# Kernel optimization log

Measured on AMD Instinct MI355X. Metric: run time of the kernel, lower is better.

The kernel has to match this reference:

```python
import jax, jax.numpy as jnp
import numpy as np

HID = 2048
NH = 16
HD = HID // NH  # 128
EPS = 1e-6
BASE = 10000.0


def _rmsnorm(x, w):
    xf = x.astype(jnp.float32)
    y = xf * jax.lax.rsqrt(jnp.mean(xf * xf, axis=-1, keepdims=True) + EPS)
    return y.astype(x.dtype) * w


def _rope_cos_sin(seq_len, dtype):
    inv_freq = 1.0 / (BASE ** (jnp.arange(0, HD, 2, dtype=jnp.float32) / HD))
    t = jnp.arange(seq_len, dtype=jnp.float32)
    freqs = jnp.outer(t, inv_freq)          # [S, HD/2]
    emb = jnp.concatenate([freqs, freqs], axis=-1)  # [S, HD]
    return jnp.cos(emb).astype(dtype), jnp.sin(emb).astype(dtype)


def _rotate_half(x):
    x1, x2 = jnp.split(x, 2, axis=-1)
    return jnp.concatenate([-x2, x1], axis=-1)


def setup_inputs() -> dict:
    key = jax.random.key(0)
    ks = jax.random.split(key, 8)
    B, S = 2, 2048
    s = 0.02
    return {
        "hidden_states": jax.random.normal(ks[0], (B, S, HID), jnp.float32),
        "Wq": jax.random.normal(ks[1], (HID, HID), jnp.float32) * s,
        "Wk": jax.random.normal(ks[2], (HID, HID), jnp.float32) * s,
        "Wv": jax.random.normal(ks[3], (HID, HID), jnp.float32) * s,
        "Wo": jax.random.normal(ks[4], (HID, HID), jnp.float32) * s,
        "w1": jax.random.normal(ks[5], (HID, HID), jnp.float32) * s,
        "w2": jax.random.normal(ks[6], (HID, HID), jnp.float32) * s,
        "w3": jax.random.normal(ks[7], (HID, HID), jnp.float32) * s,
        "ln1_w": jnp.ones((HID,), jnp.float32),
        "ln2_w": jnp.ones((HID,), jnp.float32),
    }


def reference(hidden_states, Wq, Wk, Wv, Wo, w1, w2, w3, ln1_w, ln2_w):
    B, S, _ = hidden_states.shape
    residual = hidden_states
    x = _rmsnorm(hidden_states, ln1_w)

    # projections -> [B, NH, S, HD]
    q = (x @ Wq).reshape(B, S, NH, HD).transpose(0, 2, 1, 3)
    k = (x @ Wk).reshape(B, S, NH, HD).transpose(0, 2, 1, 3)
    v = (x @ Wv).reshape(B, S, NH, HD).transpose(0, 2, 1, 3)

    cos, sin = _rope_cos_sin(S, x.dtype)  # [S, HD]
    cos = cos[None, None]  # broadcast over batch and heads
    sin = sin[None, None]
    q = q * cos + _rotate_half(q) * sin
    k = k * cos + _rotate_half(k) * sin

    scores = jnp.einsum("bhqd,bhkd->bhqk", q, k) / np.sqrt(HD).astype(np.float32)
    # no attention_mask (torch default path). fp32 softmax.
    attn = jax.nn.softmax(scores.astype(jnp.float32), axis=-1).astype(q.dtype)
    ctx = jnp.einsum("bhqk,bhkd->bhqd", attn, v)  # [B, NH, S, HD]
    ctx = ctx.transpose(0, 2, 1, 3).reshape(B, S, HID)
    attn_out = ctx @ Wo

    h = residual + attn_out
    residual = h
    y = _rmsnorm(h, ln2_w)
    mlp = (jax.nn.silu(y @ w1) * (y @ w3)) @ w2
    return residual + mlp
```

## Files before the change

kernel.cpp:

```cpp
#include <hip/hip_runtime.h>

#define HIDN 2048
#define NHEAD 16
#define HD 128
#define SEQ 2048
#define BATCH 2
#define NROWS (BATCH*SEQ)

typedef __bf16 bf16_t;
typedef bf16_t bf16x8 __attribute__((ext_vector_type(8)));
typedef float f32x4 __attribute__((ext_vector_type(4)));

#define AS1 __attribute__((address_space(1)))
#define AS3 __attribute__((address_space(3)))

__device__ __forceinline__ unsigned short f2bf(float x) {
  union { bf16_t b; unsigned short u; } cv; cv.b = (bf16_t)x; return cv.u;
}

#define MFMA16(a,b,c) __builtin_amdgcn_mfma_f32_16x16x32_bf16((a),(b),(c),0,0,0)

__device__ __forceinline__ void gload16(const void* g, void* l) {
  __builtin_amdgcn_global_load_lds((const AS1 void*)g, (AS3 void*)l, 16, 0, 0);
}

template <int TMODE>
__global__ __launch_bounds__(256) void transpose_cvt_kernel(
    const float* __restrict__ W, unsigned short* __restrict__ Wt, int half) {
  __shared__ float t[32][33];
  int bn = blockIdx.x * 32;
  int bk = blockIdx.y * 32;
  int tx = threadIdx.x & 31, ty = threadIdx.x >> 5;
#pragma unroll
  for (int i = 0; i < 4; ++i) {
    int k = bk + ty + i * 8;
    t[ty + i * 8][tx] = W[(long)k * HIDN + bn + tx];
  }
  __syncthreads();
#pragma unroll
  for (int i = 0; i < 4; ++i) {
    int n = bn + ty + i * 8;
    int dst;
    if (TMODE == 0) dst = n;
    else if (TMODE == 1) { int d = n & 127; dst = (n & ~127) | ((d & 63) << 1) | (d >> 6); }
    else dst = (n >> 4) * 32 + half * 16 + (n & 15);
    Wt[(long)dst * HIDN + bk + tx] = f2bf(t[tx][ty + i * 8]);
  }
}

__global__ void rope_table_kernel(float* __restrict__ cosT, float* __restrict__ sinT) {
  int s = blockIdx.x, d = threadIdx.x;
  float invf = powf(10000.0f, (-2.0f * (float)d) / 128.0f);
  float ang = (float)s * invf;
  cosT[s * 64 + d] = cosf(ang);
  sinT[s * 64 + d] = sinf(ang);
}

__global__ __launch_bounds__(256) void rmsnorm_kernel(
    const float* __restrict__ x, const float* __restrict__ w, unsigned short* __restrict__ out) {
  long row = blockIdx.x;
  const float* xr = x + row * HIDN;
  int c0 = threadIdx.x * 4;
  float4 v0 = *(const float4*)(xr + c0);
  float4 v1 = *(const float4*)(xr + 1024 + c0);
  float s = v0.x*v0.x + v0.y*v0.y + v0.z*v0.z + v0.w*v0.w
          + v1.x*v1.x + v1.y*v1.y + v1.z*v1.z + v1.w*v1.w;
#pragma unroll
  for (int off = 1; off < 64; off <<= 1) s += __shfl_xor(s, off);
  __shared__ float red[4];
  if ((threadIdx.x & 63) == 0) red[threadIdx.x >> 6] = s;
  __syncthreads();
  float tot = red[0] + red[1] + red[2] + red[3];
  float r = 1.0f / sqrtf(tot * (1.0f / (float)HIDN) + 1e-6f);
  float4 w0 = *(const float4*)(w + c0);
  float4 w1 = *(const float4*)(w + 1024 + c0);
  ushort4 o0, o1;
  o0.x = f2bf(v0.x * r * w0.x); o0.y = f2bf(v0.y * r * w0.y);
  o0.z = f2bf(v0.z * r * w0.z); o0.w = f2bf(v0.w * r * w0.w);
  o1.x = f2bf(v1.x * r * w1.x); o1.y = f2bf(v1.y * r * w1.y);
  o1.z = f2bf(v1.z * r * w1.z); o1.w = f2bf(v1.w * r * w1.w);
  *(ushort4*)(out + row * HIDN + c0) = o0;
  *(ushort4*)(out + row * HIDN + 1024 + c0) = o1;
}

template <int MODE>
__global__ __launch_bounds__(512, 2) void gemm256_kernel(
    const unsigned short* __restrict__ A, const unsigned short* __restrict__ Bt,
    int nbx,
    void* __restrict__ p0, void* __restrict__ p1, void* __restrict__ p2,
    const float* __restrict__ cosT, const float* __restrict__ sinT) {
  __shared__ unsigned short L[65536];
  const int tid = threadIdx.x;
  const int wave = tid >> 6, lane = tid & 63;
  const int lr = lane & 15, lkg = lane >> 4;
  const int wr = wave >> 2, wc = wave & 3;
  const int nwg = (int)gridDim.x;
  const int bid = (int)blockIdx.x;
  const int wg = (bid & 7) * (nwg >> 3) + (bid >> 3);
  const int bx = wg % nbx, by = wg / nbx;
  const long bm = (long)by * 256, bn = (long)bx * 256;
  const int srow = wave * 8 + (lane >> 3);
  const int sslot = (lane & 7) ^ (lane >> 3);
  const unsigned short* Ag = A + (bm + srow) * HIDN + sslot * 8;
  const unsigned short* Bg = Bt + (bn + srow) * HIDN + sslot * 8;
  f32x4 acc[8][4] = {};

#define STAGE256(kt2)                                                            \
  {                                                                              \
    const long ko = (long)(kt2) * 64;                                            \
    unsigned short* Ld = &L[((kt2) & 1) * 32768];                                \
    _Pragma("unroll")                                                            \
    for (int j = 0; j < 4; ++j) {                                                \
      gload16(Ag + ko + (long)j * 64 * HIDN, &Ld[(j * 64 + wave * 8) * 64]);     \
      gload16(Bg + ko + (long)j * 64 * HIDN, &Ld[16384 + (j * 64 + wave * 8) * 64]); \
    }                                                                            \
  }

  STAGE256(0);
  STAGE256(1);
  asm volatile("s_waitcnt vmcnt(8)" ::: "memory");
  __builtin_amdgcn_sched_barrier(0);
  __builtin_amdgcn_s_barrier();

  for (int kt = 0; kt < 32; ++kt) {
    const int d = kt & 1;
    const char* Lb = (const char*)L + d * 65536;
    bf16x8 bfr[4][2];
#pragma unroll
    for (int n = 0; n < 4; ++n) {
      int row = wc * 64 + n * 16 + lr;
      int x7 = row & 7;
#pragma unroll
      for (int ks = 0; ks < 2; ++ks) {
        int s = ks * 4 + lkg;
        bfr[n][ks] = *(const bf16x8*)(Lb + 32768 + row * 128 + ((s ^ x7) << 4));
      }
    }
#pragma unroll
    for (int q = 0; q < 4; ++q) {
      bf16x8 af[2][2];
#pragma unroll
      for (int mm = 0; mm < 2; ++mm) {
        int row = wr * 128 + (q * 2 + mm) * 16 + lr;
        int x7 = row & 7;
#pragma unroll
        for (int ks = 0; ks < 2; ++ks) {
          int s = ks * 4 + lkg;
          af[mm][ks] = *(const bf16x8*)(Lb + row * 128 + ((s ^ x7) << 4));
        }
      }
      __builtin_amdgcn_s_setprio(1);
#pragma unroll
      for (int mm = 0; mm < 2; ++mm)
#pragma unroll
        for (int n = 0; n < 4; ++n) {
          acc[q * 2 + mm][n] = MFMA16(af[mm][0], bfr[n][0], acc[q * 2 + mm][n]);
          acc[q * 2 + mm][n] = MFMA16(af[mm][1], bfr[n][1], acc[q * 2 + mm][n]);
        }
      __builtin_amdgcn_s_setprio(0);
    }
    if (kt == 31) break;
    asm volatile("s_waitcnt lgkmcnt(0)" ::: "memory");
    __builtin_amdgcn_sched_barrier(0);
    __builtin_amdgcn_s_barrier();
    if (kt < 30) {
      STAGE256(kt + 2);
      asm volatile("s_waitcnt vmcnt(8)" ::: "memory");
    } else {
      asm volatile("s_waitcnt vmcnt(0)" ::: "memory");
    }
    __builtin_amdgcn_sched_barrier(0);
    __builtin_amdgcn_s_barrier();
  }
#undef STAGE256

  const int gc0 = (int)bn + wc * 64;
  if (MODE == 1) {
    unsigned short* bout = (unsigned short*)p0;
#pragma unroll
    for (int m = 0; m < 8; ++m) {
      long r0 = bm + wr * 128 + m * 16 + lkg * 4;
#pragma unroll
      for (int n = 0; n < 4; n += 2) {
        int ggrp = (gc0 + n * 16) >> 5;
        long c = (long)ggrp * 16 + lr;
#pragma unroll
        for (int r = 0; r < 4; ++r) {
          float x = acc[m][n][r], g = acc[m][n + 1][r];
          float sv = x / (1.0f + __expf(-x)) * g;
          bout[(r0 + r) * 2048 + c] = f2bf(sv);
        }
      }
    }
  } else {
    int bufid = gc0 >> 11;
    unsigned short* dst = (bufid == 0) ? (unsigned short*)p0
                        : (bufid == 1) ? (unsigned short*)p1
                                       : (unsigned short*)p2;
    if (bufid == 2) {
#pragma unroll
      for (int m = 0; m < 8; ++m) {
        long r0 = bm + wr * 128 + m * 16 + lkg * 4;
#pragma unroll
        for (int n = 0; n < 4; ++n) {
          int wcol = (gc0 + n * 16 + lr) & 2047;
#pragma unroll
          for (int r = 0; r < 4; ++r) dst[(r0 + r) * 2048 + wcol] = f2bf(acc[m][n][r]);
        }
      }
    } else {
#pragma unroll
      for (int m = 0; m < 8; ++m) {
        long r0 = bm + wr * 128 + m * 16 + lkg * 4;
#pragma unroll
        for (int n = 0; n < 4; ++n) {
          int wcol = (gc0 + n * 16 + lr) & 2047;
          int f = wcol & 127, hh = wcol >> 7;
          int j = f >> 1, odd = f & 1;
          int oc = hh * 128 + (odd ? 64 : 0) + j;
#pragma unroll
          for (int r = 0; r < 4; ++r) {
            long row = r0 + r;
            int s = (int)(row & (SEQ - 1));
            float cv = cosT[s * 64 + j], sn = sinT[s * 64 + j];
            float v = acc[m][n][r];
            float o = __shfl_xor(v, 1);
            float res = odd ? (v * cv + o * sn) : (v * cv - o * sn);
            dst[row * 2048 + oc] = f2bf(res);
          }
        }
      }
    }
  }
}

template <int MODE>
__global__ __launch_bounds__(256) void gemm_kernel(
    const unsigned short* __restrict__ A, const unsigned short* __restrict__ Bt, int N,
    void* __restrict__ p0, const void* __restrict__ p1) {
  __shared__ unsigned short As[128 * 32];
  __shared__ unsigned short Bs[128 * 32];
  const int tid = threadIdx.x;
  const int lane = tid & 63, wave = tid >> 6;
  const int wm = (wave >> 1) * 64, wn = (wave & 1) * 64;
  const int lr = lane & 15, lkg = lane >> 4;
  const long bm = (long)blockIdx.y * 128, bn = (long)blockIdx.x * 128;
  f32x4 acc[4][4] = {};
  const int rA0 = wave * 32 + (lane >> 2);
  const int gs0 = (lane & 3) ^ ((rA0 >> 1) & 3);
  const int gs1 = (lane & 3) ^ (((rA0 + 16) >> 1) & 3);
  const unsigned short* Ag0 = A + (bm + rA0) * HIDN + gs0 * 8;
  const unsigned short* Ag1 = A + (bm + rA0 + 16) * HIDN + gs1 * 8;
  const unsigned short* Bg0 = Bt + (bn + rA0) * HIDN + gs0 * 8;
  const unsigned short* Bg1 = Bt + (bn + rA0 + 16) * HIDN + gs1 * 8;
  unsigned short* lA0 = &As[(wave * 32) * 32];
  unsigned short* lA1 = &As[(wave * 32 + 16) * 32];
  unsigned short* lB0 = &Bs[(wave * 32) * 32];
  unsigned short* lB1 = &Bs[(wave * 32 + 16) * 32];
  for (int k0 = 0; k0 < HIDN; k0 += 32) {
    __syncthreads();
    gload16(Ag0 + k0, lA0);
    gload16(Ag1 + k0, lA1);
    gload16(Bg0 + k0, lB0);
    gload16(Bg1 + k0, lB1);
    __syncthreads();
    bf16x8 af[4], bfr[4];
#pragma unroll
    for (int m = 0; m < 4; ++m) {
      int row = wm + m * 16 + lr;
      af[m] = *(const bf16x8*)((const char*)As + row * 64 + ((lkg ^ ((row >> 1) & 3)) << 4));
    }
#pragma unroll
    for (int n = 0; n < 4; ++n) {
      int row = wn + n * 16 + lr;
      bfr[n] = *(const bf16x8*)((const char*)Bs + row * 64 + ((lkg ^ ((row >> 1) & 3)) << 4));
    }
#pragma unroll
    for (int m = 0; m < 4; ++m)
#pragma unroll
      for (int n = 0; n < 4; ++n) acc[m][n] = MFMA16(af[m], bfr[n], acc[m][n]);
  }
  float* fout = (float*)p0;
  const float* addsrc = (const float*)p1;
#pragma unroll
  for (int m = 0; m < 4; ++m)
#pragma unroll
    for (int n = 0; n < 4; ++n) {
      long r0 = bm + wm + m * 16 + lkg * 4;
      long c = bn + wn + n * 16 + lr;
#pragma unroll
      for (int r = 0; r < 4; ++r) {
        long idx = (r0 + r) * 2048 + c;
        if (MODE == 2) fout[idx] = addsrc[idx] + acc[m][n][r];
        else fout[idx] = fout[idx] + acc[m][n][r];
      }
    }
}

__global__ __launch_bounds__(256) void flash_attn_kernel(
    const unsigned short* __restrict__ Q, const unsigned short* __restrict__ Kb,
    const unsigned short* __restrict__ Vb, unsigned short* __restrict__ O) {
  __shared__ unsigned short Ks[2][64 * 128];
  __shared__ unsigned short VtL[128 * 64];
  __shared__ unsigned short Ps[4][16][72];
  const int qt = blockIdx.x, h = blockIdx.y, b = blockIdx.z;
  const int tid = threadIdx.x, wave = tid >> 6, lane = tid & 63;
  const int lr = lane & 15, lkg = lane >> 4, lk = lkg * 8;
  const float scale = 0.08838834764831845f;
  const long rowbase = (long)b * SEQ;
  const int qrow0 = qt * 64 + wave * 16;
  bf16x8 aq[4];
#pragma unroll
  for (int ks = 0; ks < 4; ++ks)
    aq[ks] = *(const bf16x8*)(Q + (rowbase + qrow0 + lr) * HIDN + h * HD + ks * 32 + lk);
  const int kq = tid & 15, db = tid >> 4;
  const int krl = lane >> 4;
  char* vb8 = (char*)VtL;
  f32x4 acc[8] = {};
  float m_[4] = {-3.0e38f, -3.0e38f, -3.0e38f, -3.0e38f};
  float l_[4] = {0.f, 0.f, 0.f, 0.f};
  ushort4 vreg[2][4];
#pragma unroll
  for (int j = 0; j < 4; ++j) {
    int rl = wave * 16 + j * 4 + krl;
    int slot = (lane & 15) ^ (rl & 15);
    gload16(Kb + (rowbase + rl) * HIDN + h * HD + slot * 8,
            &Ks[0][(wave * 16 + j * 4) * 128]);
  }
#pragma unroll
  for (int j = 0; j < 4; ++j)
#pragma unroll
    for (int i = 0; i < 2; ++i)
      vreg[i][j] = *(const ushort4*)(Vb + (rowbase + kq * 4 + j) * HIDN + h * HD + db * 8 + i * 4);

  for (int t = 0; t < SEQ / 64; ++t) {
    asm volatile("s_waitcnt vmcnt(0)" ::: "memory");
#pragma unroll
    for (int i = 0; i < 2; ++i)
#pragma unroll
      for (int dd = 0; dd < 4; ++dd) {
        int d = db * 8 + i * 4 + dd;
        ushort4 w;
        w.x = ((const unsigned short*)&vreg[i][0])[dd];
        w.y = ((const unsigned short*)&vreg[i][1])[dd];
        w.z = ((const unsigned short*)&vreg[i][2])[dd];
        w.w = ((const unsigned short*)&vreg[i][3])[dd];
        *(ushort4*)(vb8 + d * 128 + ((kq * 8) ^ ((d & 7) << 4))) = w;
      }
    asm volatile("s_waitcnt lgkmcnt(0)" ::: "memory");
    asm volatile("s_barrier" ::: "memory");
    if (t + 1 < SEQ / 64) {
      const long kvn = (long)(t + 1) * 64;
#pragma unroll
      for (int j = 0; j < 4; ++j) {
        int rl = wave * 16 + j * 4 + krl;
        int slot = (lane & 15) ^ (rl & 15);
        gload16(Kb + (rowbase + kvn + rl) * HIDN + h * HD + slot * 8,
                &Ks[(t + 1) & 1][(wave * 16 + j * 4) * 128]);
      }
#pragma unroll
      for (int j = 0; j < 4; ++j)
#pragma unroll
        for (int i = 0; i < 2; ++i)
          vreg[i][j] = *(const ushort4*)(Vb + (rowbase + kvn + kq * 4 + j) * HIDN + h * HD + db * 8 + i * 4);
    }
    const char* ksb = (const char*)Ks[t & 1];
    f32x4 sa[4] = {};
#pragma unroll
    for (int n = 0; n < 4; ++n) {
      int row = n * 16 + lr;
#pragma unroll
      for (int ks = 0; ks < 4; ++ks) {
        bf16x8 bk = *(const bf16x8*)(ksb + row * 256 + (((ks * 4 + lkg) ^ (row & 15)) << 4));
        sa[n] = MFMA16(aq[ks], bk, sa[n]);
      }
    }
#pragma unroll
    for (int n = 0; n < 4; ++n)
#pragma unroll
      for (int r = 0; r < 4; ++r) sa[n][r] *= scale;
#pragma unroll
    for (int r = 0; r < 4; ++r) {
      float mx = fmaxf(fmaxf(sa[0][r], sa[1][r]), fmaxf(sa[2][r], sa[3][r]));
#pragma unroll
      for (int off = 1; off < 16; off <<= 1) mx = fmaxf(mx, __shfl_xor(mx, off));
      float mnew = fmaxf(m_[r], mx);
      float corr = __expf(m_[r] - mnew);
      float psum = 0.f;
#pragma unroll
      for (int n = 0; n < 4; ++n) {
        float p = __expf(sa[n][r] - mnew);
        sa[n][r] = p;
        psum += p;
      }
#pragma unroll
      for (int off = 1; off < 16; off <<= 1) psum += __shfl_xor(psum, off);
      l_[r] = l_[r] * corr + psum;
      m_[r] = mnew;
#pragma unroll
      for (int df = 0; df < 8; ++df) acc[df][r] *= corr;
    }
#pragma unroll
    for (int r = 0; r < 4; ++r)
#pragma unroll
      for (int n = 0; n < 4; ++n) Ps[wave][lkg * 4 + r][n * 16 + lr] = f2bf(sa[n][r]);
    asm volatile("s_waitcnt lgkmcnt(0)" ::: "memory");
    asm volatile("s_barrier" ::: "memory");
    bf16x8 pa0 = *(const bf16x8*)&Ps[wave][lr][lk];
    bf16x8 pa1 = *(const bf16x8*)&Ps[wave][lr][32 + lk];
#pragma unroll
    for (int df = 0; df < 8; ++df) {
      int row = df * 16 + lr;
      int sw = (row & 7) << 4;
      bf16x8 bv0 = *(const bf16x8*)(vb8 + row * 128 + ((lkg * 16) ^ sw));
      bf16x8 bv1 = *(const bf16x8*)(vb8 + row * 128 + (((4 + lkg) * 16) ^ sw));
      acc[df] = MFMA16(pa0, bv0, acc[df]);
      acc[df] = MFMA16(pa1, bv1, acc[df]);
    }
    asm volatile("s_barrier" ::: "memory");
  }
#pragma unroll
  for (int r = 0; r < 4; ++r) {
    float invl = 1.0f / l_[r];
    long orow = rowbase + qrow0 + lkg * 4 + r;
#pragma unroll
    for (int df = 0; df < 8; ++df)
      O[orow * HIDN + h * HD + df * 16 + lr] = f2bf(acc[df][r] * invl);
  }
}

extern "C" void kernel_launch(void* const* d_in, const int* in_sizes, int n_in,
                              void* d_out, int out_size, void* d_ws, size_t ws_size,
                              hipStream_t stream) {
  const float* hidden = (const float*)d_in[0];
  const float* Wq = (const float*)d_in[1];
  const float* Wk = (const float*)d_in[2];
  const float* Wv = (const float*)d_in[3];
  const float* Wo = (const float*)d_in[4];
  const float* w1 = (const float*)d_in[5];
  const float* w2 = (const float*)d_in[6];
  const float* w3 = (const float*)d_in[7];
  const float* ln1 = (const float*)d_in[8];
  const float* ln2 = (const float*)d_in[9];
  float* out = (float*)d_out;

  char* ws = (char*)d_ws;
  size_t off = 0;
  auto alloc = [&](size_t bytes) -> void* {
    void* p = ws + off;
    off += (bytes + 255) & ~(size_t)255;
    return p;
  };
  unsigned short* wblk = (unsigned short*)alloc((size_t)(2048L * 6 + 2048) * HIDN * 2);
  unsigned short* wQ = wblk;
  unsigned short* wK = wblk + (size_t)2048 * HIDN;
  unsigned short* wV = wblk + (size_t)4096 * HIDN;
  unsigned short* wO = wblk + (size_t)6144 * HIDN;
  unsigned short* wG = wblk + (size_t)8192 * HIDN;
  unsigned short* wD = wblk + (size_t)12288 * HIDN;
  unsigned short* xb   = (unsigned short*)alloc((size_t)NROWS * HIDN * 2);
  unsigned short* qb   = (unsigned short*)alloc((size_t)NROWS * HIDN * 2);
  unsigned short* kb   = (unsigned short*)alloc((size_t)NROWS * HIDN * 2);
  unsigned short* vb   = (unsigned short*)alloc((size_t)NROWS * HIDN * 2);
  unsigned short* ctxb = (unsigned short*)alloc((size_t)NROWS * HIDN * 2);
  float* cosT = (float*)alloc((size_t)SEQ * 64 * 4);
  float* sinT = (float*)alloc((size_t)SEQ * 64 * 4);
  if (off > ws_size) return;

  dim3 tgrid(HIDN / 32, HIDN / 32);
  transpose_cvt_kernel<1><<<tgrid, 256, 0, stream>>>(Wq, wQ, 0);
  transpose_cvt_kernel<1><<<tgrid, 256, 0, stream>>>(Wk, wK, 0);
  transpose_cvt_kernel<0><<<tgrid, 256, 0, stream>>>(Wv, wV, 0);
  transpose_cvt_kernel<0><<<tgrid, 256, 0, stream>>>(Wo, wO, 0);
  transpose_cvt_kernel<2><<<tgrid, 256, 0, stream>>>(w1, wG, 0);
  transpose_cvt_kernel<2><<<tgrid, 256, 0, stream>>>(w3, wG, 1);
  transpose_cvt_kernel<0><<<tgrid, 256, 0, stream>>>(w2, wD, 0);
  rope_table_kernel<<<SEQ, 64, 0, stream>>>(cosT, sinT);

  rmsnorm_kernel<<<NROWS, 256, 0, stream>>>(hidden, ln1, xb);

  gemm256_kernel<0><<<(6144 / 256) * (NROWS / 256), 512, 0, stream>>>(
      xb, wQ, 6144 / 256, qb, kb, vb, cosT, sinT);

  flash_attn_kernel<<<dim3(SEQ / 64, NHEAD, BATCH), 256, 0, stream>>>(qb, kb, vb, ctxb);

  gemm_kernel<2><<<dim3(2048 / 128, NROWS / 128), 256, 0, stream>>>(
      ctxb, wO, 2048, out, hidden);

  rmsnorm_kernel<<<NROWS, 256, 0, stream>>>(out, ln2, xb);

  gemm256_kernel<1><<<(4096 / 256) * (NROWS / 256), 512, 0, stream>>>(
      xb, wG, 4096 / 256, qb, nullptr, nullptr, nullptr, nullptr);

  gemm_kernel<3><<<dim3(2048 / 128, NROWS / 128), 256, 0, stream>>>(
      qb, wD, 2048, out, nullptr);
}
```

Before: 534.6 us.

## Transpose attention score layout for per-lane softmax and fold scale into Q

The softmax scale is folded into the Q projection epilogue, so the attention kernel no longer multiplies every score. The QK^T MFMA operands are swapped, giving the transposed score tile: each lane now holds the scores for one query row. Row max and sum then take two cross-lane shuffles instead of a 16-lane butterfly per row, and the correction and 1/l factors are redistributed with shuffles. P is written to LDS as packed 4-element stores, and the lgkmcnt wait plus barrier before the PV step are dropped. Dropping that barrier is only safe if the Ks/VtL stores issued earlier in the same iteration are synchronized elsewhere.

```diff
diff --git a/kernel.cpp b/kernel.cpp
--- a/kernel.cpp
+++ b/kernel.cpp
@@ -209,6 +209,7 @@
         }
       }
     } else {
+      const float qscale = (bufid == 0) ? 0.08838834764831845f : 1.0f;
 #pragma unroll
       for (int m = 0; m < 8; ++m) {
         long r0 = bm + wr * 128 + m * 16 + lkg * 4;
@@ -225,7 +226,7 @@
             float cv = cosT[s * 64 + j], sn = sinT[s * 64 + j];
             float v = acc[m][n][r];
             float o = __shfl_xor(v, 1);
-            float res = odd ? (v * cv + o * sn) : (v * cv - o * sn);
+            float res = (odd ? (v * cv + o * sn) : (v * cv - o * sn)) * qscale;
             dst[row * 2048 + oc] = f2bf(res);
           }
         }
@@ -306,7 +307,6 @@
   const int qt = blockIdx.x, h = blockIdx.y, b = blockIdx.z;
   const int tid = threadIdx.x, wave = tid >> 6, lane = tid & 63;
   const int lr = lane & 15, lkg = lane >> 4, lk = lkg * 8;
-  const float scale = 0.08838834764831845f;
   const long rowbase = (long)b * SEQ;
   const int qrow0 = qt * 64 + wave * 16;
   bf16x8 aq[4];
@@ -317,8 +317,7 @@
   const int krl = lane >> 4;
   char* vb8 = (char*)VtL;
   f32x4 acc[8] = {};
-  float m_[4] = {-3.0e38f, -3.0e38f, -3.0e38f, -3.0e38f};
-  float l_[4] = {0.f, 0.f, 0.f, 0.f};
+  float m_ = -3.0e38f, l_ = 0.f;
   ushort4 vreg[2][4];
 #pragma unroll
   for (int j = 0; j < 4; ++j) {
@@ -372,40 +371,45 @@
 #pragma unroll
       for (int ks = 0; ks < 4; ++ks) {
         bf16x8 bk = *(const bf16x8*)(ksb + row * 256 + (((ks * 4 + lkg) ^ (row & 15)) << 4));
-        sa[n] = MFMA16(aq[ks], bk, sa[n]);
-      }
-    }
+        sa[n] = MFMA16(bk, aq[ks], sa[n]);
+      }
+    }
+    float pmax = sa[0][0];
 #pragma unroll
     for (int n = 0; n < 4; ++n)
 #pragma unroll
-      for (int r = 0; r < 4; ++r) sa[n][r] *= scale;
-#pragma unroll
-    for (int r = 0; r < 4; ++r) {
-      float mx = fmaxf(fmaxf(sa[0][r], sa[1][r]), fmaxf(sa[2][r], sa[3][r]));
-#pragma unroll
-      for (int off = 1; off < 16; off <<= 1) mx = fmaxf(mx, __shfl_xor(mx, off));
-      float mnew = fmaxf(m_[r], mx);
-      float corr = __expf(m_[r] - mnew);
-      float psum = 0.f;
-#pragma unroll
-      for (int n = 0; n < 4; ++n) {
+      for (int r = 0; r < 4; ++r) pmax = fmaxf(pmax, sa[n][r]);
+    pmax = fmaxf(pmax, __shfl_xor(pmax, 16));
+    pmax = fmaxf(pmax, __shfl_xor(pmax, 32));
+    float mnew = fmaxf(m_, pmax);
+    float corr = __expf(m_ - mnew);
+    float psum = 0.f;
+#pragma unroll
+    for (int n = 0; n < 4; ++n)
+#pragma unroll
+      for (int r = 0; r < 4; ++r) {
         float p = __expf(sa[n][r] - mnew);
         sa[n][r] = p;
         psum += p;
       }
-#pragma unroll
-      for (int off = 1; off < 16; off <<= 1) psum += __shfl_xor(psum, off);
-      l_[r] = l_[r] * corr + psum;
-      m_[r] = mnew;
-#pragma unroll
-      for (int df = 0; df < 8; ++df) acc[df][r] *= corr;
-    }
-#pragma unroll
-    for (int r = 0; r < 4; ++r)
-#pragma unroll
-      for (int n = 0; n < 4; ++n) Ps[wave][lkg * 4 + r][n * 16 + lr] = f2bf(sa[n][r]);
-    asm volatile("s_waitcnt lgkmcnt(0)" ::: "memory");
-    asm volatile("s_barrier" ::: "memory");
+    psum += __shfl_xor(psum, 16);
+    psum += __shfl_xor(psum, 32);
+    l_ = l_ * corr + psum;
+    m_ = mnew;
+    float corr4[4];
+#pragma unroll
+    for (int r = 0; r < 4; ++r) corr4[r] = __shfl(corr, 4 * lkg + r);
+#pragma unroll
+    for (int df = 0; df < 8; ++df)
+#pragma unroll
+      for (int r = 0; r < 4; ++r) acc[df][r] *= corr4[r];
+#pragma unroll
+    for (int n = 0; n < 4; ++n) {
+      ushort4 pw;
+      pw.x = f2bf(sa[n][0]); pw.y = f2bf(sa[n][1]);
+      pw.z = f2bf(sa[n][2]); pw.w = f2bf(sa[n][3]);
+      *(ushort4*)&Ps[wave][lr][n * 16 + 4 * lkg] = pw;
+    }
     bf16x8 pa0 = *(const bf16x8*)&Ps[wave][lr][lk];
     bf16x8 pa1 = *(const bf16x8*)&Ps[wave][lr][32 + lk];
 #pragma unroll
@@ -419,13 +423,16 @@
     }
     asm volatile("s_barrier" ::: "memory");
   }
+  float invl = 1.0f / l_;
+  float invl4[4];
+#pragma unroll
+  for (int r = 0; r < 4; ++r) invl4[r] = __shfl(invl, 4 * lkg + r);
 #pragma unroll
   for (int r = 0; r < 4; ++r) {
-    float invl = 1.0f / l_[r];
     long orow = rowbase + qrow0 + lkg * 4 + r;
 #pragma unroll
     for (int df = 0; df < 8; ++df)
-      O[orow * HIDN + h * HD + df * 16 + lr] = f2bf(acc[df][r] * invl);
+      O[orow * HIDN + h * HD + df * 16 + lr] = f2bf(acc[df][r] * invl4[r]);
   }
 }
 
```

New measurement: 513.0 us. -4.0%, faster.
